# Performance work log

Measured on AMD Instinct MI355X. Metric: run time of the kernel, lower is better.

## Reference

```python
import jax, jax.numpy as jnp
import numpy as np

SIGMA = 1.0   # kernel influence distance (init kwarg)
RADIUS = 1.0  # kernel radius (kernel points live within this ball)


def setup_inputs() -> dict:
    key = jax.random.key(0)
    k0, k1, k2, k3, k4, k5 = jax.random.split(key, 6)
    N, M, H, K, Cin, Cout = 50000, 50000, 32, 15, 64, 64
    q_points = jax.random.normal(k0, (M, 3), dtype=jnp.float32)
    s_points = jax.random.normal(k1, (N, 3), dtype=jnp.float32)
    s_feats = jax.random.normal(k2, (N, Cin), dtype=jnp.float32)
    # index == N selects the padded 'fantom' point (zero features, far away)
    neighbor_indices = jax.random.randint(k3, (M, H), 0, N + 1, dtype=jnp.int64)
    kernel_points = jax.random.normal(k4, (K, 3), dtype=jnp.float32) * (0.4 * RADIUS)
    weights = jax.random.normal(k5, (K, Cin, Cout), dtype=jnp.float32) * 0.05
    return {
        'q_points': q_points,
        's_points': s_points,
        's_feats': s_feats,
        'neighbor_indices': neighbor_indices,
        'kernel_points': kernel_points,
        'weights': weights,
    }


def reference(q_points, s_points, s_feats, neighbor_indices, kernel_points, weights):
    # Pad source points with a far-away fantom point and zero features so that
    # neighbor_indices == N behaves as an empty neighbor slot.
    s_pts = jnp.concatenate([s_points, jnp.full((1, 3), 1e6, s_points.dtype)], axis=0)
    s_fts = jnp.concatenate([s_feats, jnp.zeros((1, s_feats.shape[1]), s_feats.dtype)], axis=0)

    # Gather neighbors and center on query points: (M, H, 3)
    neighbors = s_pts[neighbor_indices] - q_points[:, None, :]
    # Distances to each kernel point: (M, H, K)
    diffs = neighbors[:, :, None, :] - kernel_points[None, None, :, :]
    sq_dists = jnp.sum(diffs * diffs, axis=-1)
    # Linear kernel influence (KPConv 'linear' mode): (M, H, K)
    influence = jnp.maximum(1.0 - jnp.sqrt(sq_dists) / SIGMA, 0.0)
    # Fantom neighbors are ~1e6 away -> influence exactly 0.

    # Gather neighbor features: (M, H, Cin)
    nb_feats = s_fts[neighbor_indices]
    # Weight features by kernel influence, reduce over neighbors: (M, K, Cin)
    weighted = jnp.einsum('mhk,mhc->mkc', influence, nb_feats)
    # Apply per-kernel-point linear maps and sum over kernel points: (M, Cout)
    out = jnp.einsum('mkc,kcd->md', weighted, weights)

    # Normalize by the number of valid (non-zero-feature) neighbors.
    feat_sum = jnp.sum(nb_feats, axis=-1)               # (M, H)
    nnum = jnp.maximum(jnp.sum(feat_sum > 0.0, axis=-1), 1)  # (M,)
    return out / nnum[:, None].astype(out.dtype)
```

## Files before the change

kernel.cpp:

```cpp
#include <hip/hip_runtime.h>

#define NPTS 50000
#define MPTS 50000
#define HN 32
#define KCD 960
#define PSTRIDE 968

typedef float f32x4 __attribute__((ext_vector_type(4)));
typedef short s16x8 __attribute__((ext_vector_type(8)));

__device__ __forceinline__ unsigned short bf_rne(float x) {
    union { float f; unsigned u; } v; v.f = x;
    unsigned r = v.u + 0x7fffu + ((v.u >> 16) & 1u);
    return (unsigned short)(r >> 16);
}
__device__ __forceinline__ unsigned short bf_trunc(float x) {
    union { float f; unsigned u; } v; v.f = x;
    return (unsigned short)(v.u >> 16);
}
__device__ __forceinline__ unsigned pack_bf(float lo, float hi) {
    union { float f; unsigned u; } a, b; a.f = lo; b.f = hi;
    return __builtin_amdgcn_perm(b.u, a.u, 0x07060302u);
}

__global__ __launch_bounds__(256) void prep(const float* __restrict__ w,
                                            const float* __restrict__ feats,
                                            unsigned short* __restrict__ WT,
                                            unsigned char* __restrict__ signs) {
    int b = blockIdx.x;
    if (b < 240) {
        int t = b * 256 + threadIdx.x;
        int kc = t >> 6, d = t & 63;
        WT[d * KCD + kc] = bf_rne(w[t]);
    } else {
        int lane = threadIdx.x & 63, wv = threadIdx.x >> 6;
        int r4 = lane >> 4, c16 = lane & 15;
        int n = (b - 240) * 16 + wv * 4 + r4;
        float4 v = *(const float4*)(feats + (size_t)n * 64 + c16 * 4);
        float s = v.x + v.y + v.z + v.w;
        s += __shfl_xor(s, 1); s += __shfl_xor(s, 2);
        s += __shfl_xor(s, 4); s += __shfl_xor(s, 8);
        if (c16 == 0) signs[n] = (s > 0.f) ? 1 : 0;
    }
}

__global__ __launch_bounds__(256, 4)
void kpconv_main(const float* __restrict__ q_points,
                 const float* __restrict__ s_points,
                 const float* __restrict__ s_feats,
                 const int* __restrict__ ni,
                 const float* __restrict__ kpts,
                 const unsigned short* __restrict__ WT,
                 const unsigned char* __restrict__ signs,
                 float* __restrict__ out) {
    __shared__ __align__(16) unsigned short P_sh[16][PSTRIDE];
    __shared__ __align__(16) float rpos_sh[4][3][32];
    __shared__ int ni_sh[4][4][32];
    __shared__ float kp_sh[16][3];
    __shared__ float q_sh[16][3];
    __shared__ float inv_nnum[16];

    int tid = threadIdx.x, w = tid >> 6, lane = tid & 63;
    int m_base = blockIdx.x << 4;

    if (tid < 48) {
        kp_sh[tid / 3][tid % 3] = (tid < 45) ? kpts[tid] : 1e9f;
        q_sh[tid / 3][tid % 3] = q_points[m_base * 3 + tid];
    }
    __syncthreads();

    int h = lane & 31;
    int row = lane & 15, quad = lane >> 4, kq = quad << 3;
    int h2 = lane >> 1, half = lane & 1;

    float kx = kp_sh[row][0], ky = kp_sh[row][1], kz = kp_sh[row][2];

    float tkx[8], tky[8], tkz[8];
    #pragma unroll
    for (int j = 0; j < 8; ++j) {
        int k = half * 8 + j;
        tkx[j] = kp_sh[k][0]; tky[j] = kp_sh[k][1]; tkz[j] = kp_sh[k][2];
    }

    int idx4[4]; float rxa[4], rya[4], rza[4]; unsigned char sg4[4];
    #pragma unroll
    for (int mi = 0; mi < 4; ++mi)
        idx4[mi] = ni[(m_base + mi * 4 + w) * HN + h];
    #pragma unroll
    for (int mi = 0; mi < 4; ++mi) {
        int m_l = mi * 4 + w;
        bool valid = idx4[mi] < NPTS;
        const float* sp = s_points + (size_t)(valid ? idx4[mi] : 0) * 3;
        float px = sp[0], py = sp[1], pz = sp[2];
        unsigned char sg = signs[valid ? idx4[mi] : 0];
        rxa[mi] = (valid ? px : 1e6f) - q_sh[m_l][0];
        rya[mi] = (valid ? py : 1e6f) - q_sh[m_l][1];
        rza[mi] = (valid ? pz : 1e6f) - q_sh[m_l][2];
        sg4[mi] = valid ? sg : 0;
    }

    #pragma unroll
    for (int mi = 0; mi < 4; ++mi) {
        float rx2 = __shfl(rxa[mi], h2);
        float ry2 = __shfl(rya[mi], h2);
        float rz2 = __shfl(rza[mi], h2);
        int idx2 = __shfl(idx4[mi], h2);
        int av = 0;
        #pragma unroll
        for (int j = 0; j < 8; ++j) {
            float dx = rx2 - tkx[j], dy = ry2 - tky[j], dz = rz2 - tkz[j];
            float d2 = dx * dx + dy * dy + dz * dz;
            av |= (d2 < 1.f) ? 1 : 0;
        }
        av |= __shfl_xor(av, 1);
        bool alive = (idx2 < NPTS) && (av != 0);
        if (half == 0) ni_sh[w][mi][h2] = alive ? idx2 : NPTS;

        unsigned long long pm = __ballot((lane < 32) && (idx4[mi] < NPTS) && sg4[mi]);
        if (lane == 0) {
            int cnt = __popcll(pm);
            inv_nnum[mi * 4 + w] = 1.f / (float)(cnt < 1 ? 1 : cnt);
        }
    }

    #pragma unroll
    for (int mi = 0; mi < 4; ++mi) {
        int m_l = mi * 4 + w;
        if (lane < 32) {
            rpos_sh[w][0][h] = rxa[mi];
            rpos_sh[w][1][h] = rya[mi];
            rpos_sh[w][2][h] = rza[mi];
        }

        float g0[8], g1[8], g2[8], g3[8];
        #pragma unroll
        for (int j = 0; j < 8; ++j) {
            int idxj = ni_sh[w][mi][kq + j];
            g0[j] = 0.f; g1[j] = 0.f; g2[j] = 0.f; g3[j] = 0.f;
            if (idxj < NPTS) {
                const float* fp = s_feats + (size_t)idxj * 64 + row;
                g0[j] = fp[0]; g1[j] = fp[16]; g2[j] = fp[32]; g3[j] = fp[48];
            }
        }

        float4 ra0 = *(const float4*)&rpos_sh[w][0][kq];
        float4 ra1 = *(const float4*)&rpos_sh[w][0][kq + 4];
        float4 rb0 = *(const float4*)&rpos_sh[w][1][kq];
        float4 rb1 = *(const float4*)&rpos_sh[w][1][kq + 4];
        float4 rc0 = *(const float4*)&rpos_sh[w][2][kq];
        float4 rc1 = *(const float4*)&rpos_sh[w][2][kq + 4];
        float hx[8] = {ra0.x, ra0.y, ra0.z, ra0.w, ra1.x, ra1.y, ra1.z, ra1.w};
        float hy[8] = {rb0.x, rb0.y, rb0.z, rb0.w, rb1.x, rb1.y, rb1.z, rb1.w};
        float hz[8] = {rc0.x, rc0.y, rc0.z, rc0.w, rc1.x, rc1.y, rc1.z, rc1.w};
        float infl[8];
        #pragma unroll
        for (int j = 0; j < 8; ++j) {
            float dx = hx[j] - kx, dy = hy[j] - ky, dz = hz[j] - kz;
            float d2 = dx * dx + dy * dy + dz * dz;
            float f = 1.f - sqrtf(d2);
            infl[j] = f > 0.f ? f : 0.f;
        }
        union { unsigned u[4]; s16x8 v; } af;
        #pragma unroll
        for (int p = 0; p < 4; ++p) af.u[p] = pack_bf(infl[2 * p], infl[2 * p + 1]);

        #pragma unroll
        for (int ch = 0; ch < 4; ++ch) {
            const float* gs = (ch == 0) ? g0 : (ch == 1) ? g1 : (ch == 2) ? g2 : g3;
            union { unsigned u[4]; s16x8 v; } bf;
            #pragma unroll
            for (int p = 0; p < 4; ++p) bf.u[p] = pack_bf(gs[2 * p], gs[2 * p + 1]);
            f32x4 acc = {0.f, 0.f, 0.f, 0.f};
            acc = __builtin_amdgcn_mfma_f32_16x16x32_bf16(af.v, bf.v, acc, 0, 0, 0);
            int cc = ch * 16 + row;
            #pragma unroll
            for (int r = 0; r < 4; ++r) {
                int k2 = quad * 4 + r;
                if (k2 < 15) {
                    int col = (k2 << 6) | (cc ^ ((k2 >> 2) << 4));
                    P_sh[m_l][col] = bf_trunc(acc[r]);
                }
            }
        }
    }
    __syncthreads();

    {
        int dbase = w << 4;
        f32x4 acc = {0.f, 0.f, 0.f, 0.f};
        const unsigned short* wtp = WT + (size_t)(dbase + row) * KCD + kq;
        #pragma unroll 6
        for (int s = 0; s < 30; ++s) {
            int k = s >> 1;
            int c0 = ((s & 1) << 5) + kq;
            int cx = c0 ^ (((k >> 2) & 3) << 4);
            s16x8 a = *(const s16x8*)&P_sh[row][(k << 6) | cx];
            s16x8 b = *(const s16x8*)&wtp[s * 32];
            acc = __builtin_amdgcn_mfma_f32_16x16x32_bf16(a, b, acc, 0, 0, 0);
        }
        #pragma unroll
        for (int r = 0; r < 4; ++r) {
            int m_l = quad * 4 + r;
            out[(size_t)(m_base + m_l) * 64 + dbase + row] = acc[r] * inv_nnum[m_l];
        }
    }
}

extern "C" void kernel_launch(void* const* d_in, const int* in_sizes, int n_in,
                              void* d_out, int out_size, void* d_ws, size_t ws_size,
                              hipStream_t stream) {
    const float* q  = (const float*)d_in[0];
    const float* sp = (const float*)d_in[1];
    const float* sf = (const float*)d_in[2];
    const int*   ni = (const int*)d_in[3];
    const float* kp = (const float*)d_in[4];
    const float* wt = (const float*)d_in[5];
    float* out = (float*)d_out;

    unsigned short* WT = (unsigned short*)d_ws;
    unsigned char* signs = (unsigned char*)d_ws + 64 * KCD * 2;

    hipLaunchKernelGGL(prep, dim3(240 + NPTS / 16), dim3(256), 0, stream,
                       wt, sf, WT, signs);
    hipLaunchKernelGGL(kpconv_main, dim3(MPTS / 16), dim3(256), 0, stream,
                       q, sp, sf, ni, kp, WT, signs, out);
}
```

Measured before the change: 152.9 us.

## Replace shared index staging with shuffles, branchless zero-buffer gathers, raise occupancy

Removes the ni_sh and q_sh shared arrays. Alive neighbor indices are now passed between lanes with __shfl, and query coordinates are read directly from global memory. Feature gathers become branchless: invalid neighbors point at a zeroed 64-float buffer written by an extra prep block. It also shrinks the padded P_sh stride and raises the launch-bounds occupancy hint from 4 to 5 blocks per CU. The aim is lower LDS use and divergence so more blocks fit per CU, at the risk of register pressure or spills under the tighter bound and LDS bank conflicts from the new stride.

```diff
diff --git a/kernel.cpp b/kernel.cpp
--- a/kernel.cpp
+++ b/kernel.cpp
@@ -4,7 +4,7 @@
 #define MPTS 50000
 #define HN 32
 #define KCD 960
-#define PSTRIDE 968
+#define PSTRIDE 962
 
 typedef float f32x4 __attribute__((ext_vector_type(4)));
 typedef short s16x8 __attribute__((ext_vector_type(8)));
@@ -26,13 +26,14 @@
 __global__ __launch_bounds__(256) void prep(const float* __restrict__ w,
                                             const float* __restrict__ feats,
                                             unsigned short* __restrict__ WT,
-                                            unsigned char* __restrict__ signs) {
+                                            unsigned char* __restrict__ signs,
+                                            float* __restrict__ zerobuf) {
     int b = blockIdx.x;
     if (b < 240) {
         int t = b * 256 + threadIdx.x;
         int kc = t >> 6, d = t & 63;
         WT[d * KCD + kc] = bf_rne(w[t]);
-    } else {
+    } else if (b < 240 + NPTS / 16) {
         int lane = threadIdx.x & 63, wv = threadIdx.x >> 6;
         int r4 = lane >> 4, c16 = lane & 15;
         int n = (b - 240) * 16 + wv * 4 + r4;
@@ -41,10 +42,12 @@
         s += __shfl_xor(s, 1); s += __shfl_xor(s, 2);
         s += __shfl_xor(s, 4); s += __shfl_xor(s, 8);
         if (c16 == 0) signs[n] = (s > 0.f) ? 1 : 0;
-    }
-}
-
-__global__ __launch_bounds__(256, 4)
+    } else {
+        if (threadIdx.x < 64) zerobuf[threadIdx.x] = 0.f;
+    }
+}
+
+__global__ __launch_bounds__(256, 5)
 void kpconv_main(const float* __restrict__ q_points,
                  const float* __restrict__ s_points,
                  const float* __restrict__ s_feats,
@@ -52,21 +55,17 @@
                  const float* __restrict__ kpts,
                  const unsigned short* __restrict__ WT,
                  const unsigned char* __restrict__ signs,
+                 const float* __restrict__ zerobuf,
                  float* __restrict__ out) {
     __shared__ __align__(16) unsigned short P_sh[16][PSTRIDE];
     __shared__ __align__(16) float rpos_sh[4][3][32];
-    __shared__ int ni_sh[4][4][32];
     __shared__ float kp_sh[16][3];
-    __shared__ float q_sh[16][3];
     __shared__ float inv_nnum[16];
 
     int tid = threadIdx.x, w = tid >> 6, lane = tid & 63;
     int m_base = blockIdx.x << 4;
 
-    if (tid < 48) {
-        kp_sh[tid / 3][tid % 3] = (tid < 45) ? kpts[tid] : 1e9f;
-        q_sh[tid / 3][tid % 3] = q_points[m_base * 3 + tid];
-    }
+    if (tid < 48) kp_sh[tid / 3][tid % 3] = (tid < 45) ? kpts[tid] : 1e9f;
     __syncthreads();
 
     int h = lane & 31;
@@ -88,17 +87,18 @@
         idx4[mi] = ni[(m_base + mi * 4 + w) * HN + h];
     #pragma unroll
     for (int mi = 0; mi < 4; ++mi) {
-        int m_l = mi * 4 + w;
+        int m = m_base + mi * 4 + w;
         bool valid = idx4[mi] < NPTS;
         const float* sp = s_points + (size_t)(valid ? idx4[mi] : 0) * 3;
         float px = sp[0], py = sp[1], pz = sp[2];
         unsigned char sg = signs[valid ? idx4[mi] : 0];
-        rxa[mi] = (valid ? px : 1e6f) - q_sh[m_l][0];
-        rya[mi] = (valid ? py : 1e6f) - q_sh[m_l][1];
-        rza[mi] = (valid ? pz : 1e6f) - q_sh[m_l][2];
+        rxa[mi] = (valid ? px : 1e6f) - q_points[m * 3];
+        rya[mi] = (valid ? py : 1e6f) - q_points[m * 3 + 1];
+        rza[mi] = (valid ? pz : 1e6f) - q_points[m * 3 + 2];
         sg4[mi] = valid ? sg : 0;
     }
 
+    int idx_al[4];
     #pragma unroll
     for (int mi = 0; mi < 4; ++mi) {
         float rx2 = __shfl(rxa[mi], h2);
@@ -113,8 +113,7 @@
             av |= (d2 < 1.f) ? 1 : 0;
         }
         av |= __shfl_xor(av, 1);
-        bool alive = (idx2 < NPTS) && (av != 0);
-        if (half == 0) ni_sh[w][mi][h2] = alive ? idx2 : NPTS;
+        idx_al[mi] = ((idx2 < NPTS) && (av != 0)) ? idx2 : NPTS;
 
         unsigned long long pm = __ballot((lane < 32) && (idx4[mi] < NPTS) && sg4[mi]);
         if (lane == 0) {
@@ -135,12 +134,10 @@
         float g0[8], g1[8], g2[8], g3[8];
         #pragma unroll
         for (int j = 0; j < 8; ++j) {
-            int idxj = ni_sh[w][mi][kq + j];
-            g0[j] = 0.f; g1[j] = 0.f; g2[j] = 0.f; g3[j] = 0.f;
-            if (idxj < NPTS) {
-                const float* fp = s_feats + (size_t)idxj * 64 + row;
-                g0[j] = fp[0]; g1[j] = fp[16]; g2[j] = fp[32]; g3[j] = fp[48];
-            }
+            int idxj = __shfl(idx_al[mi], 2 * (kq + j));
+            const float* fp = (idxj < NPTS) ? (s_feats + (size_t)idxj * 64) : zerobuf;
+            fp += row;
+            g0[j] = fp[0]; g1[j] = fp[16]; g2[j] = fp[32]; g3[j] = fp[48];
         }
 
         float4 ra0 = *(const float4*)&rpos_sh[w][0][kq];
@@ -219,9 +216,10 @@
 
     unsigned short* WT = (unsigned short*)d_ws;
     unsigned char* signs = (unsigned char*)d_ws + 64 * KCD * 2;
-
-    hipLaunchKernelGGL(prep, dim3(240 + NPTS / 16), dim3(256), 0, stream,
-                       wt, sf, WT, signs);
+    float* zerobuf = (float*)((char*)d_ws + 64 * KCD * 2 + 50048);
+
+    hipLaunchKernelGGL(prep, dim3(240 + NPTS / 16 + 1), dim3(256), 0, stream,
+                       wt, sf, WT, signs, zerobuf);
     hipLaunchKernelGGL(kpconv_main, dim3(MPTS / 16), dim3(256), 0, stream,
-                       q, sp, sf, ni, kp, WT, signs, out);
-}
+                       q, sp, sf, ni, kp, WT, signs, zerobuf, out);
+}
```

New measurement: 161.0 us. 1.05x slower.
